# Performance work log

Measured on AMD Instinct MI355X. Metric: run time of the kernel, lower is better.

## Reference

```python
import jax, jax.numpy as jnp
import numpy as np

B, C_LEN, Q_LEN, DIM = 8, 2048, 512, 512


def setup_inputs() -> dict:
    key = jax.random.key(0)
    ks = jax.random.split(key, 6)
    s = 1.0 / np.sqrt(DIM).astype(np.float32)
    return {
        "C": jax.random.normal(ks[0], (C_LEN, B, DIM), jnp.float32),
        "Q": jax.random.normal(ks[1], (Q_LEN, B, DIM), jnp.float32),
        "C_mask": jnp.ones((C_LEN, B), jnp.int32),
        "Q_mask": jnp.ones((Q_LEN, B), jnp.int32),
        "Wq": jax.random.normal(ks[2], (DIM, DIM), jnp.float32) * s,
        "bq": jnp.zeros((DIM,), jnp.float32),
        "w1": jax.random.normal(ks[3], (DIM,), jnp.float32) * s,
        "w2": jax.random.normal(ks[4], (DIM,), jnp.float32) * s,
        "w3": jax.random.normal(ks[5], (DIM,), jnp.float32) * s,
        "b": jnp.zeros((), jnp.float32),
    }


def reference(C, Q, C_mask, Q_mask, Wq, bq, w1, w2, w3, b):
    # seq-first -> batch-first
    Cb = jnp.transpose(C, (1, 0, 2))   # [B, c_len, d]
    Qb = jnp.transpose(Q, (1, 0, 2))   # [B, q_len, d]
    Cm = C_mask.T                      # [B, c_len]
    Qm = Q_mask.T                      # [B, q_len]

    Qp = Qb @ Wq + bq                  # Q_linear: [B, q_len, d]

    # Trilinear score S[b,i,j] = w1.C_i + w2.Q_j + w3.(C_i*Q_j) + b
    # (decomposed form of Linear(cat(C, Q, C*Q)) -> avoids [B,c,q,3d] blowup)
    S = ((Cb @ w1)[:, :, None]
         + (Qp @ w2)[:, None, :]
         + jnp.einsum('bid,bjd->bij', Cb * w3, Qp)
         + b)                          # [B, c_len, q_len]

    neg_inf = jnp.float32(-jnp.inf)
    S_row = jax.nn.softmax(jnp.where(Qm[:, None, :] == 0, neg_inf, S), axis=2)
    S_col = jax.nn.softmax(jnp.where(Cm[:, :, None] == 0, neg_inf, S), axis=1)

    A = S_row @ Qp                                        # [B, c_len, d]
    # (S_row @ S_col^T) @ C == S_row @ (S_col^T @ C), cheaper association
    Bm = S_row @ jnp.einsum('bij,bid->bjd', S_col, Cb)    # [B, c_len, d]

    CQ = jnp.concatenate((Cb, A, Cb * A, Cb * Bm), axis=-1)  # [B, c_len, 4d]
    return jnp.transpose(CQ, (1, 0, 2))                      # [c_len, B, 4d]
```

## Files before the change

kernel.cpp:

```cpp
#include <hip/hip_runtime.h>
#include <math.h>

constexpr int BB = 8;
constexpr int CL = 2048;
constexpr int QL = 512;
constexpr int DM = 512;

typedef short          bf16x8 __attribute__((ext_vector_type(8)));
typedef unsigned short us8    __attribute__((ext_vector_type(8)));
typedef float          f32x4  __attribute__((ext_vector_type(4)));

__device__ __forceinline__ unsigned short f2b(float f) {
  union { float f; unsigned u; } v; v.f = f;
  return (unsigned short)((v.u + 0x7FFFu + ((v.u >> 16) & 1u)) >> 16);
}

enum { G_QP = 0, G_S = 1, G_TT = 2, G_A = 3, G_BM = 4 };

template <int MODE, int WR, int WC>
__global__ __launch_bounds__(WR * WC * 64) void mgemm(
    const unsigned short* __restrict__ A, int sA, size_t batA,
    const unsigned short* __restrict__ B, int sB, size_t batB,
    int K,
    float* __restrict__ Of, unsigned short* __restrict__ Ob,
    int sD, size_t batD,
    const float* __restrict__ e1, const float* __restrict__ e2,
    const float* __restrict__ e3)
{
  const int tid = threadIdx.x, b = blockIdx.z;
  const int wave = tid >> 6, lane = tid & 63;
  const int wr = wave / WC, wc = wave % WC;
  const int m0 = blockIdx.x * (WR * 64) + wr * 64;
  const int n0 = blockIdx.y * (WC * 64) + wc * 64;
  const int l15 = lane & 15, lk8 = (lane >> 4) * 8;

  const unsigned short* ap = A + batA * b + (size_t)(m0 + l15) * sA + lk8;
  const unsigned short* bp = B + batB * b + (size_t)(n0 + l15) * sB + lk8;

  f32x4 acc[4][4];
  #pragma unroll
  for (int mr = 0; mr < 4; mr++)
    #pragma unroll
    for (int nc = 0; nc < 4; nc++) acc[mr][nc] = (f32x4){0.f, 0.f, 0.f, 0.f};

  for (int k0 = 0; k0 < K; k0 += 32) {
    bf16x8 af[4], bf[4];
    #pragma unroll
    for (int mr = 0; mr < 4; mr++)
      af[mr] = *(const bf16x8*)(ap + (size_t)mr * 16 * sA + k0);
    #pragma unroll
    for (int nc = 0; nc < 4; nc++)
      bf[nc] = *(const bf16x8*)(bp + (size_t)nc * 16 * sB + k0);
    #pragma unroll
    for (int mr = 0; mr < 4; mr++)
      #pragma unroll
      for (int nc = 0; nc < 4; nc++)
        acc[mr][nc] = __builtin_amdgcn_mfma_f32_16x16x32_bf16(
            af[mr], bf[nc], acc[mr][nc], 0, 0, 0);
  }

  const int r0 = (lane >> 4) * 4;
  #pragma unroll
  for (int mr = 0; mr < 4; mr++) {
    #pragma unroll
    for (int nc = 0; nc < 4; nc++) {
      const int col = n0 + nc * 16 + l15;
      float addc = 0.f;
      if constexpr (MODE == G_QP) addc = e2[col];
      if constexpr (MODE == G_S)  addc = e2[b * QL + col] + e3[0];
      #pragma unroll
      for (int r = 0; r < 4; r++) {
        const int row = m0 + mr * 16 + r0 + r;
        float v = acc[mr][nc][r] + addc;
        if constexpr (MODE == G_S) {
          v += e1[b * CL + row];
          Of[batD * b + (size_t)row * sD + col] = v;
        } else if constexpr (MODE == G_QP) {
          Of[batD * b + (size_t)row * sD + col] = v;
          Ob[batD * b + (size_t)row * sD + col] = f2b(v);
        } else if constexpr (MODE == G_TT) {
          Ob[batD * b + (size_t)row * sD + col] = f2b(v);
        } else {
          const size_t obase = ((size_t)row * BB + b) * (4 * DM) + col;
          const float c = e1[((size_t)row * BB + b) * DM + col];
          if constexpr (MODE == G_A) {
            Of[obase] = c;
            Of[obase + DM] = v;
            Of[obase + 2 * DM] = c * v;
          } else {
            Of[obase + 3 * DM] = c * v;
          }
        }
      }
    }
  }
}

__global__ __launch_bounds__(256) void cast8(const float* __restrict__ src,
                                             unsigned short* __restrict__ dst)
{
  const int g = blockIdx.x * 256 + threadIdx.x;
  const float4 v0 = *((const float4*)src + g * 2);
  const float4 v1 = *((const float4*)src + g * 2 + 1);
  us8 r = {f2b(v0.x), f2b(v0.y), f2b(v0.z), f2b(v0.w),
           f2b(v1.x), f2b(v1.y), f2b(v1.z), f2b(v1.w)};
  *((us8*)dst + g) = r;
}

__global__ __launch_bounds__(256) void build_cw3c(
    const float* __restrict__ C, const float* __restrict__ w3,
    const float* __restrict__ w1, unsigned short* __restrict__ dst,
    float* __restrict__ c1)
{
  const int g = blockIdx.x * 256 + threadIdx.x;
  const int orow = g >> 6, d0 = (g & 63) * 8;
  const int b = orow >> 11, i = orow & 2047;
  const float* s = C + ((size_t)i * BB + b) * DM + d0;
  const float4 v0 = *(const float4*)s, v1 = *(const float4*)(s + 4);
  const float4 w30 = *(const float4*)(w3 + d0), w31 = *(const float4*)(w3 + d0 + 4);
  const float4 w10 = *(const float4*)(w1 + d0), w11 = *(const float4*)(w1 + d0 + 4);
  us8 r = {f2b(v0.x * w30.x), f2b(v0.y * w30.y), f2b(v0.z * w30.z), f2b(v0.w * w30.w),
           f2b(v1.x * w31.x), f2b(v1.y * w31.y), f2b(v1.z * w31.z), f2b(v1.w * w31.w)};
  *(us8*)(dst + (size_t)orow * DM + d0) = r;
  float sdot = v0.x * w10.x + v0.y * w10.y + v0.z * w10.z + v0.w * w10.w +
               v1.x * w11.x + v1.y * w11.y + v1.z * w11.z + v1.w * w11.w;
  #pragma unroll
  for (int off = 32; off; off >>= 1) sdot += __shfl_xor(sdot, off);
  if ((g & 63) == 0) c1[orow] = sdot;
}

__global__ __launch_bounds__(256) void transbf(const float* __restrict__ src,
                                               unsigned short* __restrict__ dst,
                                               int sSrc, int sDst,
                                               size_t batSrc, size_t batDst)
{
  __shared__ float t[64][65];
  const int b = blockIdx.z;
  const int r0 = blockIdx.x * 64, c0 = blockIdx.y * 64;
  const int tx = threadIdx.x & 63, ty = threadIdx.x >> 6;
  const float* S = src + batSrc * b;
  unsigned short* D = dst + batDst * b;
  #pragma unroll
  for (int rr = 0; rr < 16; rr++) {
    const int r = ty * 16 + rr;
    t[r][tx] = S[(size_t)(r0 + r) * sSrc + c0 + tx];
  }
  __syncthreads();
  #pragma unroll
  for (int rr = 0; rr < 16; rr++) {
    const int c = ty * 16 + rr;
    D[(size_t)(c0 + c) * sDst + r0 + tx] = f2b(t[tx][c]);
  }
}

__global__ __launch_bounds__(256) void row_softmax(
    const float* __restrict__ S, const int* __restrict__ qm,
    unsigned short* __restrict__ dst)
{
  const int rid = blockIdx.x * 4 + (threadIdx.x >> 6);
  const int lane = threadIdx.x & 63;
  const int b = rid >> 11;
  const float* row = S + (size_t)rid * QL;
  const float4 v0 = *(const float4*)(row + lane * 8);
  const float4 v1 = *(const float4*)(row + lane * 8 + 4);
  const float va[8] = {v0.x, v0.y, v0.z, v0.w, v1.x, v1.y, v1.z, v1.w};
  int mk[8];
  float m = -INFINITY;
  #pragma unroll
  for (int e = 0; e < 8; e++) {
    mk[e] = qm[(lane * 8 + e) * BB + b];
    if (mk[e]) m = fmaxf(m, va[e]);
  }
  #pragma unroll
  for (int off = 32; off; off >>= 1) m = fmaxf(m, __shfl_xor(m, off));
  float s = 0.f;
  #pragma unroll
  for (int e = 0; e < 8; e++) if (mk[e]) s += expf(va[e] - m);
  #pragma unroll
  for (int off = 32; off; off >>= 1) s += __shfl_xor(s, off);
  const float iv = 1.f / s;
  us8 r;
  #pragma unroll
  for (int e = 0; e < 8; e++)
    r[e] = mk[e] ? f2b(expf(va[e] - m) * iv) : (unsigned short)0;
  *(us8*)(dst + (size_t)rid * QL + lane * 8) = r;
}

__global__ __launch_bounds__(256) void build_pcolt(
    const float* __restrict__ Sm, const int* __restrict__ cm,
    const float* __restrict__ cmax, const float* __restrict__ cinv,
    unsigned short* __restrict__ dst)
{
  __shared__ float t[64][65];
  const int b = blockIdx.z;
  const int i0 = blockIdx.x * 64, j0 = blockIdx.y * 64;
  const int tx = threadIdx.x & 63, ty = threadIdx.x >> 6;
  const float* S = Sm + (size_t)b * CL * QL;
  #pragma unroll
  for (int rr = 0; rr < 16; rr++) {
    const int i = ty * 16 + rr;
    t[i][tx] = S[(size_t)(i0 + i) * QL + j0 + tx];
  }
  __syncthreads();
  const int cmv = cm[(i0 + tx) * BB + b];
  #pragma unroll
  for (int rr = 0; rr < 16; rr++) {
    const int j = j0 + ty * 16 + rr;
    const float mj = cmax[b * QL + j], ivj = cinv[b * QL + j];
    const float v = t[tx][ty * 16 + rr];
    dst[(size_t)b * QL * CL + (size_t)j * CL + i0 + tx] =
        cmv ? f2b(expf(v - mj) * ivj) : (unsigned short)0;
  }
}

__global__ __launch_bounds__(256) void rowdot(const float* __restrict__ src,
                                              const float* __restrict__ w,
                                              float* __restrict__ out)
{
  const int rid = blockIdx.x * 4 + (threadIdx.x >> 6);
  const int lane = threadIdx.x & 63;
  const float* row = src + (size_t)rid * DM;
  float4 v0 = *(const float4*)(row + lane * 8);
  float4 v1 = *(const float4*)(row + lane * 8 + 4);
  float4 w0 = *(const float4*)(w + lane * 8);
  float4 w1 = *(const float4*)(w + lane * 8 + 4);
  float s = v0.x * w0.x + v0.y * w0.y + v0.z * w0.z + v0.w * w0.w +
            v1.x * w1.x + v1.y * w1.y + v1.z * w1.z + v1.w * w1.w;
  #pragma unroll
  for (int off = 32; off; off >>= 1) s += __shfl_xor(s, off);
  if (lane == 0) out[rid] = s;
}

constexpr int CH = 16;

__global__ __launch_bounds__(256) void col_part(const float* __restrict__ S,
    const int* __restrict__ cm, float* __restrict__ pmax, float* __restrict__ psum)
{
  const int t = blockIdx.x * 256 + threadIdx.x;
  const int ch = blockIdx.y;
  const int b = t >> 9, j = t & 511;
  const float* col = S + (size_t)b * CL * QL + j;
  float m = -INFINITY, s = 0.f;
  const int i0 = ch * (CL / CH);
  for (int i = 0; i < CL / CH; i++) {
    const int ig = i0 + i;
    const float v = col[(size_t)ig * QL];
    if (cm[ig * BB + b]) {
      const float nm = fmaxf(m, v);
      s = s * expf(m - nm) + expf(v - nm);
      m = nm;
    }
  }
  pmax[ch * 4096 + t] = m;
  psum[ch * 4096 + t] = s;
}

__global__ __launch_bounds__(256) void col_comb(const float* __restrict__ pmax,
    const float* __restrict__ psum, float* __restrict__ cmax, float* __restrict__ cinv)
{
  const int t = blockIdx.x * 256 + threadIdx.x;
  float m = -INFINITY;
  #pragma unroll
  for (int ch = 0; ch < CH; ch++) m = fmaxf(m, pmax[ch * 4096 + t]);
  float s = 0.f;
  #pragma unroll
  for (int ch = 0; ch < CH; ch++) {
    const float pm = pmax[ch * 4096 + t];
    if (pm > -INFINITY) s += psum[ch * 4096 + t] * expf(pm - m);
  }
  cmax[t] = m;
  cinv[t] = 1.f / s;
}

extern "C" void kernel_launch(void* const* d_in, const int* in_sizes, int n_in,
                              void* d_out, int out_size, void* d_ws, size_t ws_size,
                              hipStream_t stream)
{
  const float* C  = (const float*)d_in[0];
  const float* Q  = (const float*)d_in[1];
  const int*   Cm = (const int*)d_in[2];
  const int*   Qm = (const int*)d_in[3];
  const float* Wq = (const float*)d_in[4];
  const float* bq = (const float*)d_in[5];
  const float* w1 = (const float*)d_in[6];
  const float* w2 = (const float*)d_in[7];
  const float* w3 = (const float*)d_in[8];
  const float* bs = (const float*)d_in[9];
  float* out = (float*)d_out;
  float* ws  = (float*)d_ws;

  float* S    = ws;
  float* Qp   = ws + 8388608;
  float* c1   = ws + 10485760;
  float* q2   = ws + 10502144;
  float* cmax = ws + 10506240;
  float* cinv = ws + 10510336;
  float* pmax = ws + 10514432;
  float* psum = ws + 10579968;
  unsigned short* bfp   = (unsigned short*)(ws + 10645504);
  unsigned short* Qb    = bfp;
  unsigned short* Ttb   = bfp;
  unsigned short* Wqt   = bfp + 2097152;
  unsigned short* Cw3b  = bfp + 2359296;
  unsigned short* Prow  = bfp + 2359296;
  unsigned short* Qpb   = bfp + 10747904;
  unsigned short* Qpbt  = bfp + 12845056;
  unsigned short* PcolT = bfp + 14942208;
  unsigned short* Cbt   = (unsigned short*)S;

  cast8<<<1024, 256, 0, stream>>>(Q, Qb);
  transbf<<<dim3(8, 8, 1), 256, 0, stream>>>(Wq, Wqt, DM, DM, 0, 0);
  build_cw3c<<<4096, 256, 0, stream>>>(C, w3, w1, Cw3b, c1);

  mgemm<G_QP, 1, 2><<<dim3(8, 4, BB), 128, 0, stream>>>(
      Qb, BB * DM, DM, Wqt, DM, 0, DM,
      Qp, Qpb, DM, (size_t)QL * DM, nullptr, bq, nullptr);
  transbf<<<dim3(8, 8, BB), 256, 0, stream>>>(Qp, Qpbt, DM, QL,
                                              (size_t)QL * DM, (size_t)DM * QL);
  rowdot<<<1024, 256, 0, stream>>>(Qp, w2, q2);

  mgemm<G_S, 2, 2><<<dim3(16, 4, BB), 256, 0, stream>>>(
      Cw3b, DM, (size_t)CL * DM, Qpb, DM, (size_t)QL * DM, DM,
      S, nullptr, QL, (size_t)CL * QL, c1, q2, bs);

  row_softmax<<<4096, 256, 0, stream>>>(S, Qm, Prow);

  col_part<<<dim3(16, CH), 256, 0, stream>>>(S, Cm, pmax, psum);
  col_comb<<<16, 256, 0, stream>>>(pmax, psum, cmax, cinv);
  build_pcolt<<<dim3(32, 8, BB), 256, 0, stream>>>(S, Cm, cmax, cinv, PcolT);

  transbf<<<dim3(32, 8, BB), 256, 0, stream>>>(C, Cbt, BB * DM, CL,
                                               DM, (size_t)DM * CL);

  mgemm<G_TT, 1, 2><<<dim3(8, 4, BB), 128, 0, stream>>>(
      Cbt, CL, (size_t)DM * CL, PcolT, CL, (size_t)QL * CL, CL,
      nullptr, Ttb, QL, (size_t)DM * QL, nullptr, nullptr, nullptr);

  mgemm<G_A, 2, 2><<<dim3(16, 4, BB), 256, 0, stream>>>(
      Prow, QL, (size_t)CL * QL, Qpbt, QL, (size_t)DM * QL, QL,
      out, nullptr, 0, 0, C, nullptr, nullptr);

  mgemm<G_BM, 2, 2><<<dim3(16, 4, BB), 256, 0, stream>>>(
      Prow, QL, (size_t)CL * QL, Ttb, QL, (size_t)DM * QL, QL,
      out, nullptr, 0, 0, C, nullptr, nullptr);
}
```

Measured before the change: 478.0 us.

## Fuse score GEMM with row softmax and column softmax partial statistics

Replaces the separate S GEMM, row_softmax and col_part kernels with one s_mega kernel. Each 512-thread block computes a full 64x512 row strip of S, does the row softmax through shared-memory reductions to write Prow directly, and produces per-strip column max/sum partials (CH raised to 32). This removes two full passes reading S back from memory and two launches. In exchange the GEMM grid shrinks to 256 blocks with no LDS operand sharing, register pressure goes up, and some expf calls become the faster, less accurate __expf.

```diff
diff --git a/kernel.cpp b/kernel.cpp
--- a/kernel.cpp
+++ b/kernel.cpp
@@ -15,7 +15,7 @@
   return (unsigned short)((v.u + 0x7FFFu + ((v.u >> 16) & 1u)) >> 16);
 }
 
-enum { G_QP = 0, G_S = 1, G_TT = 2, G_A = 3, G_BM = 4 };
+enum { G_QP = 0, G_TT = 1, G_A = 2, G_BM = 3 };
 
 template <int MODE, int WR, int WC>
 __global__ __launch_bounds__(WR * WC * 64) void mgemm(
@@ -24,8 +24,7 @@
     int K,
     float* __restrict__ Of, unsigned short* __restrict__ Ob,
     int sD, size_t batD,
-    const float* __restrict__ e1, const float* __restrict__ e2,
-    const float* __restrict__ e3)
+    const float* __restrict__ e1, const float* __restrict__ e2)
 {
   const int tid = threadIdx.x, b = blockIdx.z;
   const int wave = tid >> 6, lane = tid & 63;
@@ -67,15 +66,11 @@
       const int col = n0 + nc * 16 + l15;
       float addc = 0.f;
       if constexpr (MODE == G_QP) addc = e2[col];
-      if constexpr (MODE == G_S)  addc = e2[b * QL + col] + e3[0];
       #pragma unroll
       for (int r = 0; r < 4; r++) {
         const int row = m0 + mr * 16 + r0 + r;
         float v = acc[mr][nc][r] + addc;
-        if constexpr (MODE == G_S) {
-          v += e1[b * CL + row];
-          Of[batD * b + (size_t)row * sD + col] = v;
-        } else if constexpr (MODE == G_QP) {
+        if constexpr (MODE == G_QP) {
           Of[batD * b + (size_t)row * sD + col] = v;
           Ob[batD * b + (size_t)row * sD + col] = f2b(v);
         } else if constexpr (MODE == G_TT) {
@@ -96,6 +91,172 @@
   }
 }
 
+__global__ __launch_bounds__(512) void s_mega(
+    const unsigned short* __restrict__ Aop,
+    const unsigned short* __restrict__ Bop,
+    const float* __restrict__ c1, const float* __restrict__ q2,
+    const float* __restrict__ bsc,
+    const int* __restrict__ qm, const int* __restrict__ cm,
+    float* __restrict__ S, unsigned short* __restrict__ Prow,
+    float* __restrict__ pmax, float* __restrict__ psum)
+{
+  __shared__ float red[64][9];
+  __shared__ float redF[64];
+  const int b = blockIdx.z;
+  const int m0 = blockIdx.x * 64;
+  const int wave = threadIdx.x >> 6, lane = threadIdx.x & 63;
+  const int n0 = wave * 64;
+  const int l15 = lane & 15, g4 = lane >> 4, lk8 = g4 * 8;
+
+  const unsigned short* ap = Aop + (size_t)b * CL * DM + (size_t)(m0 + l15) * DM + lk8;
+  const unsigned short* bp = Bop + (size_t)b * QL * DM + (size_t)(n0 + l15) * DM + lk8;
+
+  f32x4 acc[4][4];
+  #pragma unroll
+  for (int mr = 0; mr < 4; mr++)
+    #pragma unroll
+    for (int nc = 0; nc < 4; nc++) acc[mr][nc] = (f32x4){0.f, 0.f, 0.f, 0.f};
+
+  for (int k0 = 0; k0 < DM; k0 += 32) {
+    bf16x8 af[4], bf[4];
+    #pragma unroll
+    for (int mr = 0; mr < 4; mr++)
+      af[mr] = *(const bf16x8*)(ap + (size_t)mr * 16 * DM + k0);
+    #pragma unroll
+    for (int nc = 0; nc < 4; nc++)
+      bf[nc] = *(const bf16x8*)(bp + (size_t)nc * 16 * DM + k0);
+    #pragma unroll
+    for (int mr = 0; mr < 4; mr++)
+      #pragma unroll
+      for (int nc = 0; nc < 4; nc++)
+        acc[mr][nc] = __builtin_amdgcn_mfma_f32_16x16x32_bf16(
+            af[mr], bf[nc], acc[mr][nc], 0, 0, 0);
+  }
+
+  const float sb = bsc[0];
+  float q2c[4];
+  int qmk[4];
+  #pragma unroll
+  for (int nc = 0; nc < 4; nc++) {
+    const int col = n0 + nc * 16 + l15;
+    q2c[nc] = q2[b * QL + col] + sb;
+    qmk[nc] = qm[col * BB + b];
+  }
+  float c1r[4][4];
+  int cmk[4][4];
+  #pragma unroll
+  for (int mr = 0; mr < 4; mr++)
+    #pragma unroll
+    for (int r = 0; r < 4; r++) {
+      const int row = m0 + mr * 16 + g4 * 4 + r;
+      c1r[mr][r] = c1[b * CL + row];
+      cmk[mr][r] = cm[row * BB + b];
+    }
+  #pragma unroll
+  for (int mr = 0; mr < 4; mr++)
+    #pragma unroll
+    for (int nc = 0; nc < 4; nc++) {
+      const int col = n0 + nc * 16 + l15;
+      #pragma unroll
+      for (int r = 0; r < 4; r++) {
+        const int row = m0 + mr * 16 + g4 * 4 + r;
+        const float v = acc[mr][nc][r] + q2c[nc] + c1r[mr][r];
+        acc[mr][nc][r] = v;
+        S[(size_t)(b * CL + row) * QL + col] = v;
+      }
+    }
+
+  #pragma unroll
+  for (int mr = 0; mr < 4; mr++)
+    #pragma unroll
+    for (int r = 0; r < 4; r++) {
+      float m = -INFINITY;
+      #pragma unroll
+      for (int nc = 0; nc < 4; nc++)
+        if (qmk[nc]) m = fmaxf(m, acc[mr][nc][r]);
+      #pragma unroll
+      for (int off = 1; off < 16; off <<= 1) m = fmaxf(m, __shfl_xor(m, off));
+      if (l15 == 0) red[mr * 16 + g4 * 4 + r][wave] = m;
+    }
+  __syncthreads();
+  if (threadIdx.x < 64) {
+    float m = -INFINITY;
+    #pragma unroll
+    for (int w = 0; w < 8; w++) m = fmaxf(m, red[threadIdx.x][w]);
+    redF[threadIdx.x] = m;
+  }
+  __syncthreads();
+  float ev[4][4][4];
+  #pragma unroll
+  for (int mr = 0; mr < 4; mr++)
+    #pragma unroll
+    for (int r = 0; r < 4; r++) {
+      const float M = redF[mr * 16 + g4 * 4 + r];
+      float s = 0.f;
+      #pragma unroll
+      for (int nc = 0; nc < 4; nc++) {
+        const float e = qmk[nc] ? __expf(acc[mr][nc][r] - M) : 0.f;
+        ev[mr][nc][r] = e;
+        s += e;
+      }
+      #pragma unroll
+      for (int off = 1; off < 16; off <<= 1) s += __shfl_xor(s, off);
+      if (l15 == 0) red[mr * 16 + g4 * 4 + r][wave] = s;
+    }
+  __syncthreads();
+  if (threadIdx.x < 64) {
+    float s = 0.f;
+    #pragma unroll
+    for (int w = 0; w < 8; w++) s += red[threadIdx.x][w];
+    redF[threadIdx.x] = 1.f / s;
+  }
+  __syncthreads();
+  #pragma unroll
+  for (int mr = 0; mr < 4; mr++)
+    #pragma unroll
+    for (int r = 0; r < 4; r++) {
+      const int row = m0 + mr * 16 + g4 * 4 + r;
+      const float iv = redF[mr * 16 + g4 * 4 + r];
+      #pragma unroll
+      for (int nc = 0; nc < 4; nc++) {
+        const int col = n0 + nc * 16 + l15;
+        Prow[(size_t)(b * CL + row) * QL + col] =
+            qmk[nc] ? f2b(ev[mr][nc][r] * iv) : (unsigned short)0;
+      }
+    }
+
+  #pragma unroll
+  for (int nc = 0; nc < 4; nc++) {
+    float m = -INFINITY, s = 0.f;
+    #pragma unroll
+    for (int mr = 0; mr < 4; mr++)
+      #pragma unroll
+      for (int r = 0; r < 4; r++)
+        if (cmk[mr][r]) {
+          const float x = acc[mr][nc][r];
+          const float nm = fmaxf(m, x);
+          s = s * __expf(m - nm) + __expf(x - nm);
+          m = nm;
+        }
+    #pragma unroll
+    for (int off = 16; off < 64; off <<= 1) {
+      const float om = __shfl_xor(m, off);
+      const float os = __shfl_xor(s, off);
+      const float nm = fmaxf(m, om);
+      if (nm > -INFINITY)
+        s = s * __expf(m - nm) + os * __expf(om - nm);
+      else
+        s = 0.f;
+      m = nm;
+    }
+    if (g4 == 0) {
+      const int idx = blockIdx.x * (BB * QL) + b * QL + n0 + nc * 16 + l15;
+      pmax[idx] = m;
+      psum[idx] = s;
+    }
+  }
+}
+
 __global__ __launch_bounds__(256) void cast8(const float* __restrict__ src,
                                              unsigned short* __restrict__ dst)
 {
@@ -153,39 +314,6 @@
   }
 }
 
-__global__ __launch_bounds__(256) void row_softmax(
-    const float* __restrict__ S, const int* __restrict__ qm,
-    unsigned short* __restrict__ dst)
-{
-  const int rid = blockIdx.x * 4 + (threadIdx.x >> 6);
-  const int lane = threadIdx.x & 63;
-  const int b = rid >> 11;
-  const float* row = S + (size_t)rid * QL;
-  const float4 v0 = *(const float4*)(row + lane * 8);
-  const float4 v1 = *(const float4*)(row + lane * 8 + 4);
-  const float va[8] = {v0.x, v0.y, v0.z, v0.w, v1.x, v1.y, v1.z, v1.w};
-  int mk[8];
-  float m = -INFINITY;
-  #pragma unroll
-  for (int e = 0; e < 8; e++) {
-    mk[e] = qm[(lane * 8 + e) * BB + b];
-    if (mk[e]) m = fmaxf(m, va[e]);
-  }
-  #pragma unroll
-  for (int off = 32; off; off >>= 1) m = fmaxf(m, __shfl_xor(m, off));
-  float s = 0.f;
-  #pragma unroll
-  for (int e = 0; e < 8; e++) if (mk[e]) s += expf(va[e] - m);
-  #pragma unroll
-  for (int off = 32; off; off >>= 1) s += __shfl_xor(s, off);
-  const float iv = 1.f / s;
-  us8 r;
-  #pragma unroll
-  for (int e = 0; e < 8; e++)
-    r[e] = mk[e] ? f2b(expf(va[e] - m) * iv) : (unsigned short)0;
-  *(us8*)(dst + (size_t)rid * QL + lane * 8) = r;
-}
-
 __global__ __launch_bounds__(256) void build_pcolt(
     const float* __restrict__ Sm, const int* __restrict__ cm,
     const float* __restrict__ cmax, const float* __restrict__ cinv,
@@ -209,7 +337,7 @@
     const float mj = cmax[b * QL + j], ivj = cinv[b * QL + j];
     const float v = t[tx][ty * 16 + rr];
     dst[(size_t)b * QL * CL + (size_t)j * CL + i0 + tx] =
-        cmv ? f2b(expf(v - mj) * ivj) : (unsigned short)0;
+        cmv ? f2b(__expf(v - mj) * ivj) : (unsigned short)0;
   }
 }
 
@@ -231,29 +359,7 @@
   if (lane == 0) out[rid] = s;
 }
 
-constexpr int CH = 16;
-
-__global__ __launch_bounds__(256) void col_part(const float* __restrict__ S,
-    const int* __restrict__ cm, float* __restrict__ pmax, float* __restrict__ psum)
-{
-  const int t = blockIdx.x * 256 + threadIdx.x;
-  const int ch = blockIdx.y;
-  const int b = t >> 9, j = t & 511;
-  const float* col = S + (size_t)b * CL * QL + j;
-  float m = -INFINITY, s = 0.f;
-  const int i0 = ch * (CL / CH);
-  for (int i = 0; i < CL / CH; i++) {
-    const int ig = i0 + i;
-    const float v = col[(size_t)ig * QL];
-    if (cm[ig * BB + b]) {
-      const float nm = fmaxf(m, v);
-      s = s * expf(m - nm) + expf(v - nm);
-      m = nm;
-    }
-  }
-  pmax[ch * 4096 + t] = m;
-  psum[ch * 4096 + t] = s;
-}
+constexpr int CH = 32;
 
 __global__ __launch_bounds__(256) void col_comb(const float* __restrict__ pmax,
     const float* __restrict__ psum, float* __restrict__ cmax, float* __restrict__ cinv)
@@ -266,7 +372,7 @@
   #pragma unroll
   for (int ch = 0; ch < CH; ch++) {
     const float pm = pmax[ch * 4096 + t];
-    if (pm > -INFINITY) s += psum[ch * 4096 + t] * expf(pm - m);
+    if (pm > -INFINITY) s += psum[ch * 4096 + t] * __expf(pm - m);
   }
   cmax[t] = m;
   cinv[t] = 1.f / s;
@@ -296,8 +402,8 @@
   float* cmax = ws + 10506240;
   float* cinv = ws + 10510336;
   float* pmax = ws + 10514432;
-  float* psum = ws + 10579968;
-  unsigned short* bfp   = (unsigned short*)(ws + 10645504);
+  float* psum = ws + 10645504;
+  unsigned short* bfp   = (unsigned short*)(ws + 10776576);
   unsigned short* Qb    = bfp;
   unsigned short* Ttb   = bfp;
   unsigned short* Wqt   = bfp + 2097152;
@@ -314,18 +420,14 @@
 
   mgemm<G_QP, 1, 2><<<dim3(8, 4, BB), 128, 0, stream>>>(
       Qb, BB * DM, DM, Wqt, DM, 0, DM,
-      Qp, Qpb, DM, (size_t)QL * DM, nullptr, bq, nullptr);
+      Qp, Qpb, DM, (size_t)QL * DM, nullptr, bq);
   transbf<<<dim3(8, 8, BB), 256, 0, stream>>>(Qp, Qpbt, DM, QL,
                                               (size_t)QL * DM, (size_t)DM * QL);
   rowdot<<<1024, 256, 0, stream>>>(Qp, w2, q2);
 
-  mgemm<G_S, 2, 2><<<dim3(16, 4, BB), 256, 0, stream>>>(
-      Cw3b, DM, (size_t)CL * DM, Qpb, DM, (size_t)QL * DM, DM,
-      S, nullptr, QL, (size_t)CL * QL, c1, q2, bs);
-
-  row_softmax<<<4096, 256, 0, stream>>>(S, Qm, Prow);
-
-  col_part<<<dim3(16, CH), 256, 0, stream>>>(S, Cm, pmax, psum);
+  s_mega<<<dim3(32, 1, BB), 512, 0, stream>>>(
+      Cw3b, Qpb, c1, q2, bs, Qm, Cm, S, Prow, pmax, psum);
+
   col_comb<<<16, 256, 0, stream>>>(pmax, psum, cmax, cinv);
   build_pcolt<<<dim3(32, 8, BB), 256, 0, stream>>>(S, Cm, cmax, cinv, PcolT);
 
@@ -334,13 +436,13 @@
 
   mgemm<G_TT, 1, 2><<<dim3(8, 4, BB), 128, 0, stream>>>(
       Cbt, CL, (size_t)DM * CL, PcolT, CL, (size_t)QL * CL, CL,
-      nullptr, Ttb, QL, (size_t)DM * QL, nullptr, nullptr, nullptr);
+      nullptr, Ttb, QL, (size_t)DM * QL, nullptr, nullptr);
 
   mgemm<G_A, 2, 2><<<dim3(16, 4, BB), 256, 0, stream>>>(
       Prow, QL, (size_t)CL * QL, Qpbt, QL, (size_t)DM * QL, QL,
-      out, nullptr, 0, 0, C, nullptr, nullptr);
+      out, nullptr, 0, 0, C, nullptr);
 
   mgemm<G_BM, 2, 2><<<dim3(16, 4, BB), 256, 0, stream>>>(
       Prow, QL, (size_t)CL * QL, Ttb, QL, (size_t)DM * QL, QL,
-      out, nullptr, 0, 0, C, nullptr, nullptr);
-}
+      out, nullptr, 0, 0, C, nullptr);
+}
```

Result: faster. 414.8 us (-13.2%).
